# Kernel optimization log

Measured on AMD Instinct MI355X. Metric: run time of the kernel, lower is better.

The kernel has to match this reference:

```python
import jax, jax.numpy as jnp
import numpy as np

N = 8192      # num nodes
D = 256       # input feature dim (num_embeddings)
F_OUT = 128   # out_channels
B = 4096      # lookup batch size


def setup_inputs() -> dict:
    key = jax.random.key(0)
    k1, k2, k3, k4 = jax.random.split(key, 4)
    x = jax.random.randint(k1, (B,), 0, N)                      # node ids for final lookup
    adj = jax.random.randint(k2, (N, N), 0, 2).astype(jnp.int32)  # dense 0/1 adjacency
    embedding = jax.random.normal(k3, (N, D), dtype=jnp.float32)
    xavier = 1.414 * (6.0 / (D + F_OUT)) ** 0.5
    W = jax.random.uniform(k4, (D, F_OUT), minval=-xavier, maxval=xavier, dtype=jnp.float32)
    return {"x": x, "adj": adj, "embedding": embedding, "W": W}


def reference(x, adj, embedding, W):
    Wh = embedding @ W                                   # [N, F_OUT]
    mask = adj > 0
    maskf = mask.astype(Wh.dtype)
    # per-row neighbor mean of Wh (vectorized form of the python row loop)
    deg = jnp.maximum(jnp.sum(maskf, axis=1), 1.0)       # guard; random adj has deg>0
    neigh_mean = (maskf @ Wh) / deg[:, None]             # [N, F_OUT]
    alpha = jnp.sum(Wh * neigh_mean, axis=1)             # [N], Wh[i] . mean(neighbors)
    e = Wh @ Wh.T + alpha[:, None]                       # similarity + row-wise query term
    att = jax.nn.softmax(jnp.where(mask, e, jnp.asarray(-9e15, e.dtype)), axis=1)
    # dropout is identity in eval mode (p effectively 0)
    h_prime = att @ Wh                                   # [N, F_OUT]
    emb_out = jax.nn.elu(h_prime)                        # concat=True branch
    out = emb_out[x]                                     # F.embedding lookup, [B, F_OUT]
    nrm = jnp.linalg.norm(out, axis=1, keepdims=True)
    return out / jnp.maximum(nrm, 1e-12)                 # F.normalize (L2, eps=1e-12)
```

## Files before the change

kernel.cpp:

```cpp
#include <hip/hip_runtime.h>

#define NN 8192
#define DD 256
#define FF 128
#define BB 4096
#define NSPLIT 8
#define KCHUNK (NN / NSPLIT)
#define NITER (KCHUNK / 64)

typedef unsigned short ushortT;
typedef __attribute__((ext_vector_type(8))) short bf16x8;
typedef __attribute__((ext_vector_type(4))) float f32x4;

__device__ __forceinline__ ushortT f2bf(float f) {
  unsigned u = __float_as_uint(f);
  return (ushortT)((u + 0x7FFFu + ((u >> 16) & 1u)) >> 16);
}
__device__ __forceinline__ float bf2f(ushortT h) {
  return __uint_as_float(((unsigned)h) << 16);
}


__global__ __launch_bounds__(256) void init_kernel(int* flags, int* cnt) {
  int i = blockIdx.x * 256 + threadIdx.x;
  flags[i] = 0;
  if (i == 0) *cnt = 0;
}

__global__ __launch_bounds__(256) void scatter_kernel(const int* __restrict__ x, int* flags) {
  int b = blockIdx.x * 256 + threadIdx.x;
  flags[x[b]] = 1;
}

__global__ __launch_bounds__(256) void compact_kernel(const int* __restrict__ flags, int* cnt,
                                                      int* list, int* slot) {
  int i = blockIdx.x * 256 + threadIdx.x;
  if (flags[i]) {
    int pos = atomicAdd(cnt, 1);
    list[pos] = i;
    slot[i] = pos;
  }
}


__global__ __launch_bounds__(256) void pack_kernel(const int* __restrict__ adj,
                                                   const int* __restrict__ list,
                                                   const int* __restrict__ cntp,
                                                   unsigned* __restrict__ pk) {
  const int s = blockIdx.x >> 2;
  const int kc = (blockIdx.x & 3) * 2048;
  if (s >= *cntp) return;
  const int w = threadIdx.x >> 6, l = threadIdx.x & 63;
  const int* base = adj + (size_t)list[s] * NN + kc + w * 512;
  unsigned long long* dst = (unsigned long long*)(pk + s * 256 + (kc >> 5) + w * 16);
#pragma unroll
  for (int i = 0; i < 8; ++i) {
    unsigned long long b = __ballot(base[i * 64 + l] > 0);
    if (l == 0) dst[i] = b;
  }
}


__global__ __launch_bounds__(256) void wh_kernel(const float* __restrict__ emb,
                                                 const float* __restrict__ W,
                                                 ushortT* __restrict__ Whh,
                                                 ushortT* __restrict__ Whl) {
  __shared__ float Es[32 * 65];
  __shared__ float Ws[64 * 128];
  const int t = threadIdx.x;
  const int r0 = blockIdx.x * 32;
  const int rg = t >> 5;
  const int cg = t & 31;
  float4 acc[4] = {{0,0,0,0},{0,0,0,0},{0,0,0,0},{0,0,0,0}};
  for (int kc = 0; kc < DD; kc += 64) {
    __syncthreads();
    for (int i = 0; i < 8; ++i) {
      int idx = t + 256 * i;
      int r = idx >> 6, k = idx & 63;
      Es[r * 65 + k] = emb[(r0 + r) * DD + kc + k];
    }
    for (int i = 0; i < 8; ++i) {
      int idx = t + 256 * i;
      int kr = idx >> 5, c4 = (idx & 31) * 4;
      *(float4*)&Ws[kr * 128 + c4] = *(const float4*)&W[(kc + kr) * 128 + c4];
    }
    __syncthreads();
    for (int k = 0; k < 64; ++k) {
      float4 b = *(const float4*)&Ws[k * 128 + cg * 4];
#pragma unroll
      for (int i = 0; i < 4; ++i) {
        float a = Es[(rg * 4 + i) * 65 + k];
        acc[i].x += a * b.x; acc[i].y += a * b.y;
        acc[i].z += a * b.z; acc[i].w += a * b.w;
      }
    }
  }
#pragma unroll
  for (int i = 0; i < 4; ++i) {
    int row = r0 + rg * 4 + i;
    float v[4] = {acc[i].x, acc[i].y, acc[i].z, acc[i].w};
    ushort4 hh, ll;
    ushortT* hp = (ushortT*)&hh;
    ushortT* lp = (ushortT*)&ll;
#pragma unroll
    for (int k = 0; k < 4; ++k) {
      ushortT h = f2bf(v[k]);
      hp[k] = h;
      lp[k] = f2bf(v[k] - bf2f(h));
    }
    *(ushort4*)&Whh[row * FF + cg * 4] = hh;
    *(ushort4*)&Whl[row * FF + cg * 4] = ll;
  }
}


__global__ __launch_bounds__(256) void transpose_kernel(const ushortT* __restrict__ A,
                                                        ushortT* __restrict__ At) {
  __shared__ ushortT tile[64 * 72];
  const int t = threadIdx.x;
  const int r0 = (blockIdx.x >> 1) * 64, c0 = (blockIdx.x & 1) * 64;
#pragma unroll
  for (int i = 0; i < 2; ++i) {
    int idx = t + 256 * i;
    int r = idx >> 3, cb = idx & 7;
    *(bf16x8*)&tile[r * 72 + ((cb ^ ((r >> 3) & 7)) * 8)] =
        *(const bf16x8*)&A[(size_t)(r0 + r) * FF + c0 + cb * 8];
  }
  __syncthreads();
#pragma unroll
  for (int i = 0; i < 2; ++i) {
    int idx = t + 256 * i;
    int f = idx >> 3, r8 = idx & 7;
    bf16x8 v;
#pragma unroll
    for (int u = 0; u < 8; ++u) {
      int row = r8 * 8 + u;
      v[u] = (short)tile[row * 72 + (((f >> 3) ^ ((row >> 3) & 7)) * 8) + (f & 7)];
    }
    *(bf16x8*)&At[(size_t)(c0 + f) * NN + r0 + r8 * 8] = v;
  }
}


__global__ __launch_bounds__(256) void attn_kernel(
    const ushortT* __restrict__ Whh, const ushortT* __restrict__ Whl,
    const ushortT* __restrict__ WhT, const unsigned* __restrict__ pk,
    const int* __restrict__ list, const int* __restrict__ cntp,
    float* __restrict__ Opart, float* __restrict__ mpart, float* __restrict__ lpart) {
  __shared__ short Kh[2][64 * 128];
  __shared__ short Kl[2][64 * 128];
  __shared__ short Ps[4][16 * 72];
  __shared__ int nid[64];

  const int cnt = *cntp;
  const int qblk = blockIdx.x >> 3, chunk = blockIdx.x & 7;
  const int q0 = qblk * 64;
  if (q0 >= cnt) return;

  const int t = threadIdx.x;
  if (t < 64) nid[t] = list[min(q0 + t, cnt - 1)];
  __syncthreads();

  const int w = t >> 6, l = t & 63, quad = l >> 4, c = l & 15;

  const size_t qr = (size_t)nid[w * 16 + c] * FF;
  bf16x8 qh[4], ql[4];
#pragma unroll
  for (int ks = 0; ks < 4; ++ks) {
    qh[ks] = *(const bf16x8*)(Whh + qr + ks * 32 + quad * 8);
    ql[ks] = *(const bf16x8*)(Whl + qr + ks * 32 + quad * 8);
  }
  int prow[4];
#pragma unroll
  for (int r = 0; r < 4; ++r) prow[r] = min(q0 + w * 16 + quad * 4 + r, cnt - 1);

  float m[4], lr[4];
#pragma unroll
  for (int r = 0; r < 4; ++r) { m[r] = -1e30f; lr[r] = 0.f; }
  f32x4 O[8] = {{0,0,0,0},{0,0,0,0},{0,0,0,0},{0,0,0,0},
                {0,0,0,0},{0,0,0,0},{0,0,0,0},{0,0,0,0}};

  const int kt0 = chunk * KCHUNK;

  bf16x8 sgh[4], sgl[4];
  {
    const ushortT* gh = Whh + (size_t)kt0 * FF;
    const ushortT* gl = Whl + (size_t)kt0 * FF;
#pragma unroll
    for (int i = 0; i < 4; ++i) {
      int idx = t + 256 * i;
      sgh[i] = *(const bf16x8*)(gh + idx * 8);
      sgl[i] = *(const bf16x8*)(gl + idx * 8);
    }
#pragma unroll
    for (int i = 0; i < 4; ++i) {
      int idx = t + 256 * i;
      int r = idx >> 4, cb = idx & 15;
      int off = r * 128 + ((cb ^ (r & 7)) * 8);
      *(bf16x8*)&Kh[0][off] = sgh[i];
      *(bf16x8*)&Kl[0][off] = sgl[i];
    }
  }

  for (int it = 0; it < NITER; ++it) {
    const int kt = kt0 + it * 64;
    const int cur = it & 1;
    if (it + 1 < NITER) {
      const ushortT* gh = Whh + (size_t)(kt + 64) * FF;
      const ushortT* gl = Whl + (size_t)(kt + 64) * FF;
#pragma unroll
      for (int i = 0; i < 4; ++i) {
        int idx = t + 256 * i;
        sgh[i] = *(const bf16x8*)(gh + idx * 8);
        sgl[i] = *(const bf16x8*)(gl + idx * 8);
      }
    }
    unsigned mw0[4], mw1[4];
#pragma unroll
    for (int r = 0; r < 4; ++r) {
      uint2 mm = *(const uint2*)(pk + (size_t)prow[r] * 256 + (kt >> 5));
      mw0[r] = mm.x; mw1[r] = mm.y;
    }
    __syncthreads();

    f32x4 sacc[4];
#pragma unroll
    for (int nt = 0; nt < 4; ++nt) {
      const int rb = (nt * 16 + c) * 128;
      f32x4 a = {0, 0, 0, 0};
#pragma unroll
      for (int ks = 0; ks < 4; ++ks) {
        const int off = rb + (((ks * 4 + quad) ^ (c & 7)) * 8);
        bf16x8 bh = *(const bf16x8*)&Kh[cur][off];
        bf16x8 bl = *(const bf16x8*)&Kl[cur][off];
        a = __builtin_amdgcn_mfma_f32_16x16x32_bf16(qh[ks], bh, a, 0, 0, 0);
        a = __builtin_amdgcn_mfma_f32_16x16x32_bf16(ql[ks], bh, a, 0, 0, 0);
        a = __builtin_amdgcn_mfma_f32_16x16x32_bf16(qh[ks], bl, a, 0, 0, 0);
      }
      sacc[nt] = a;
    }

    float rmax[4];
#pragma unroll
    for (int r = 0; r < 4; ++r) {
      float v = -1e30f;
#pragma unroll
      for (int nt = 0; nt < 4; ++nt) {
        unsigned bit = ((nt < 2 ? mw0[r] : mw1[r]) >> ((nt & 1) * 16 + c)) & 1u;
        v = fmaxf(v, bit ? sacc[nt][r] : -1e30f);
      }
      rmax[r] = v;
    }
#pragma unroll
    for (int mk = 1; mk <= 8; mk <<= 1)
#pragma unroll
      for (int r = 0; r < 4; ++r) rmax[r] = fmaxf(rmax[r], __shfl_xor(rmax[r], mk, 16));
    float sc[4], psum[4];
#pragma unroll
    for (int r = 0; r < 4; ++r) {
      float nm = fmaxf(m[r], rmax[r]);
      sc[r] = __expf(m[r] - nm);
      m[r] = nm;
      psum[r] = 0.f;
    }
#pragma unroll
    for (int nt = 0; nt < 4; ++nt)
#pragma unroll
      for (int r = 0; r < 4; ++r) {
        unsigned bit = ((nt < 2 ? mw0[r] : mw1[r]) >> ((nt & 1) * 16 + c)) & 1u;
        float p = bit ? __expf(sacc[nt][r] - m[r]) : 0.f;
        ushortT pb = f2bf(p);
        Ps[w][(quad * 4 + r) * 72 + nt * 16 + c] = (short)pb;
        psum[r] += bf2f(pb);
      }
#pragma unroll
    for (int mk = 1; mk <= 8; mk <<= 1)
#pragma unroll
      for (int r = 0; r < 4; ++r) psum[r] += __shfl_xor(psum[r], mk, 16);
#pragma unroll
    for (int r = 0; r < 4; ++r) lr[r] = lr[r] * sc[r] + psum[r];

#pragma unroll
    for (int ft = 0; ft < 8; ++ft)
#pragma unroll
      for (int r = 0; r < 4; ++r) O[ft][r] *= sc[r];
    bf16x8 pa[2];
#pragma unroll
    for (int ks2 = 0; ks2 < 2; ++ks2)
      pa[ks2] = *(const bf16x8*)&Ps[w][c * 72 + ks2 * 32 + quad * 8];
#pragma unroll
    for (int ft = 0; ft < 8; ++ft) {
      const ushortT* vp = WhT + (size_t)(ft * 16 + c) * NN + kt + quad * 8;
#pragma unroll
      for (int ks2 = 0; ks2 < 2; ++ks2) {
        bf16x8 vb = *(const bf16x8*)(vp + ks2 * 32);
        O[ft] = __builtin_amdgcn_mfma_f32_16x16x32_bf16(pa[ks2], vb, O[ft], 0, 0, 0);
      }
    }

    if (it + 1 < NITER) {
#pragma unroll
      for (int i = 0; i < 4; ++i) {
        int idx = t + 256 * i;
        int r = idx >> 4, cb = idx & 15;
        int off = r * 128 + ((cb ^ (r & 7)) * 8);
        *(bf16x8*)&Kh[1 - cur][off] = sgh[i];
        *(bf16x8*)&Kl[1 - cur][off] = sgl[i];
      }
    }
  }

  float* Op = Opart + (size_t)chunk * 4096 * FF;
#pragma unroll
  for (int ft = 0; ft < 8; ++ft)
#pragma unroll
    for (int r = 0; r < 4; ++r)
      Op[(size_t)(q0 + w * 16 + quad * 4 + r) * FF + ft * 16 + c] = O[ft][r];
  if (c == 0) {
#pragma unroll
    for (int r = 0; r < 4; ++r) {
      mpart[chunk * 4096 + q0 + w * 16 + quad * 4 + r] = m[r];
      lpart[chunk * 4096 + q0 + w * 16 + quad * 4 + r] = lr[r];
    }
  }
}


__global__ __launch_bounds__(128) void combine_kernel(
    const float* __restrict__ Opart, const float* __restrict__ mpart,
    const float* __restrict__ lpart, float* __restrict__ h) {
  const int r = blockIdx.x;
  const int t = threadIdx.x;
  float mstar = -1e30f;
#pragma unroll
  for (int c = 0; c < NSPLIT; ++c) mstar = fmaxf(mstar, mpart[c * 4096 + r]);
  float lstar = 0.f, acc = 0.f;
#pragma unroll
  for (int c = 0; c < NSPLIT; ++c) {
    float wgt = __expf(mpart[c * 4096 + r] - mstar);
    lstar += wgt * lpart[c * 4096 + r];
    acc += wgt * Opart[((size_t)c * 4096 + r) * FF + t];
  }
  float v = acc / fmaxf(lstar, 1e-30f);
  h[r * FF + t] = v > 0.f ? v : expm1f(v);
}


__global__ __launch_bounds__(128) void out_kernel(const int* __restrict__ x,
                                                  const int* __restrict__ slot,
                                                  const float* __restrict__ h,
                                                  float* __restrict__ out) {
  const int b = blockIdx.x, t = threadIdx.x;
  const int s = slot[x[b]];
  float v = h[s * FF + t];
  float ss = v * v;
#pragma unroll
  for (int wd = 1; wd <= 32; wd <<= 1) ss += __shfl_xor(ss, wd);
  __shared__ float red[2];
  if ((t & 63) == 0) red[t >> 6] = ss;
  __syncthreads();
  float tot = red[0] + red[1];
  float scale = 1.f / fmaxf(sqrtf(tot), 1e-12f);
  out[b * FF + t] = v * scale;
}


extern "C" void kernel_launch(void* const* d_in, const int* in_sizes, int n_in,
                              void* d_out, int out_size, void* d_ws, size_t ws_size,
                              hipStream_t stream) {
  const int*   x   = (const int*)d_in[0];
  const int*   adj = (const int*)d_in[1];
  const float* emb = (const float*)d_in[2];
  const float* W   = (const float*)d_in[3];
  float* out = (float*)d_out;

  char* base = (char*)d_ws;
  ushortT* Whh = (ushortT*)(base);
  ushortT* Whl = (ushortT*)(base + 2097152);
  float*   h   = (float*)(base + 2097152);
  ushortT* WhT = (ushortT*)(base + 4194304);
  float* Opart = (float*)(base + 6291456);
  float* mpart = (float*)(base + 23068672);
  float* lpart = (float*)(base + 23199744);
  unsigned* pk = (unsigned*)(base + 23330816);
  int*   flags = (int*)(base + 27525120);
  int*   list  = (int*)(base + 27557888);
  int*   slot  = (int*)(base + 27574272);
  int*   cnt   = (int*)(base + 27607040);
  (void)in_sizes; (void)n_in; (void)out_size; (void)ws_size;

  hipLaunchKernelGGL(init_kernel,      dim3(NN / 256), dim3(256), 0, stream, flags, cnt);
  hipLaunchKernelGGL(scatter_kernel,   dim3(BB / 256), dim3(256), 0, stream, x, flags);
  hipLaunchKernelGGL(compact_kernel,   dim3(NN / 256), dim3(256), 0, stream, flags, cnt, list, slot);
  hipLaunchKernelGGL(pack_kernel,      dim3(4096 * 4), dim3(256), 0, stream, adj, list, cnt, pk);
  hipLaunchKernelGGL(wh_kernel,        dim3(NN / 32),  dim3(256), 0, stream, emb, W, Whh, Whl);
  hipLaunchKernelGGL(transpose_kernel, dim3((NN / 64) * 2), dim3(256), 0, stream, Whh, WhT);
  hipLaunchKernelGGL(attn_kernel,      dim3((BB / 64) * NSPLIT), dim3(256), 0, stream,
                     Whh, Whl, WhT, pk, list, cnt, Opart, mpart, lpart);
  hipLaunchKernelGGL(combine_kernel,   dim3(4096), dim3(128), 0, stream, Opart, mpart, lpart, h);
  hipLaunchKernelGGL(out_kernel,       dim3(BB),   dim3(128), 0, stream, x, slot, h, out);
}
```

Before: 463.8 us.

## Switch attention to fp16 split-precision, drop low key half, double key splits

Replaces the bf16 hi/lo split of Wh with fp16 hi/lo. The QK^T product now uses two MFMAs per step (q_hi·k_hi and q_lo·k_hi) instead of three, and the Kl shared-memory buffer and its global loads are removed. NSPLIT goes from 8 to 16 to give more blocks, launch_bounds now asks for 3 blocks per CU, and the workspace offsets grow to fit the larger partial buffers. Risks are fp16 range/overflow and lower key precision in the logits, plus more partial-result combine traffic.

After: 475.3 us. +2.5%, slower.

```diff
diff --git a/kernel.cpp b/kernel.cpp
--- a/kernel.cpp
+++ b/kernel.cpp
@@ -4,20 +4,20 @@
 #define DD 256
 #define FF 128
 #define BB 4096
-#define NSPLIT 8
+#define NSPLIT 16
 #define KCHUNK (NN / NSPLIT)
 #define NITER (KCHUNK / 64)
 
 typedef unsigned short ushortT;
-typedef __attribute__((ext_vector_type(8))) short bf16x8;
+typedef _Float16 f16;
+typedef __attribute__((ext_vector_type(8))) _Float16 f16x8;
 typedef __attribute__((ext_vector_type(4))) float f32x4;
 
-__device__ __forceinline__ ushortT f2bf(float f) {
-  unsigned u = __float_as_uint(f);
-  return (ushortT)((u + 0x7FFFu + ((u >> 16) & 1u)) >> 16);
-}
-__device__ __forceinline__ float bf2f(ushortT h) {
-  return __uint_as_float(((unsigned)h) << 16);
+__device__ __forceinline__ ushortT f2h_bits(float f) {
+  f16 h = (f16)f; ushortT u; __builtin_memcpy(&u, &h, 2); return u;
+}
+__device__ __forceinline__ float h_bits2f(ushortT u) {
+  f16 h; __builtin_memcpy(&h, &u, 2); return (float)h;
 }
 
 
@@ -104,9 +104,9 @@
     ushortT* lp = (ushortT*)&ll;
 #pragma unroll
     for (int k = 0; k < 4; ++k) {
-      ushortT h = f2bf(v[k]);
+      ushortT h = f2h_bits(v[k]);
       hp[k] = h;
-      lp[k] = f2bf(v[k] - bf2f(h));
+      lp[k] = f2h_bits(v[k] - h_bits2f(h));
     }
     *(ushort4*)&Whh[row * FF + cg * 4] = hh;
     *(ushort4*)&Whl[row * FF + cg * 4] = ll;
@@ -123,52 +123,68 @@
   for (int i = 0; i < 2; ++i) {
     int idx = t + 256 * i;
     int r = idx >> 3, cb = idx & 7;
-    *(bf16x8*)&tile[r * 72 + ((cb ^ ((r >> 3) & 7)) * 8)] =
-        *(const bf16x8*)&A[(size_t)(r0 + r) * FF + c0 + cb * 8];
+    *(ushort4*)&tile[r * 72 + ((cb ^ ((r >> 3) & 7)) * 8)] =
+        *(const ushort4*)&A[(size_t)(r0 + r) * FF + c0 + cb * 8];
+    *(ushort4*)&tile[r * 72 + ((cb ^ ((r >> 3) & 7)) * 8) + 4] =
+        *(const ushort4*)&A[(size_t)(r0 + r) * FF + c0 + cb * 8 + 4];
   }
   __syncthreads();
 #pragma unroll
   for (int i = 0; i < 2; ++i) {
     int idx = t + 256 * i;
     int f = idx >> 3, r8 = idx & 7;
-    bf16x8 v;
+    ushortT v[8];
 #pragma unroll
     for (int u = 0; u < 8; ++u) {
       int row = r8 * 8 + u;
-      v[u] = (short)tile[row * 72 + (((f >> 3) ^ ((row >> 3) & 7)) * 8) + (f & 7)];
-    }
-    *(bf16x8*)&At[(size_t)(c0 + f) * NN + r0 + r8 * 8] = v;
-  }
-}
-
-
-__global__ __launch_bounds__(256) void attn_kernel(
+      v[u] = tile[row * 72 + (((f >> 3) ^ ((row >> 3) & 7)) * 8) + (f & 7)];
+    }
+    *(ushort4*)&At[(size_t)(c0 + f) * NN + r0 + r8 * 8] = *(ushort4*)&v[0];
+    *(ushort4*)&At[(size_t)(c0 + f) * NN + r0 + r8 * 8 + 4] = *(ushort4*)&v[4];
+  }
+}
+
+
+__global__ __launch_bounds__(256, 3) void attn_kernel(
     const ushortT* __restrict__ Whh, const ushortT* __restrict__ Whl,
     const ushortT* __restrict__ WhT, const unsigned* __restrict__ pk,
     const int* __restrict__ list, const int* __restrict__ cntp,
     float* __restrict__ Opart, float* __restrict__ mpart, float* __restrict__ lpart) {
   __shared__ short Kh[2][64 * 128];
-  __shared__ short Kl[2][64 * 128];
   __shared__ short Ps[4][16 * 72];
   __shared__ int nid[64];
 
   const int cnt = *cntp;
-  const int qblk = blockIdx.x >> 3, chunk = blockIdx.x & 7;
+  const int qblk = blockIdx.x >> 4, chunk = blockIdx.x & 15;
   const int q0 = qblk * 64;
   if (q0 >= cnt) return;
 
   const int t = threadIdx.x;
   if (t < 64) nid[t] = list[min(q0 + t, cnt - 1)];
+  const int kt0 = chunk * KCHUNK;
+
+  f16x8 sg[4];
+#pragma unroll
+  for (int i = 0; i < 4; ++i) {
+    int idx = t + 256 * i;
+    sg[i] = *(const f16x8*)(Whh + (size_t)(kt0 + (idx >> 4)) * FF + (idx & 15) * 8);
+  }
   __syncthreads();
+#pragma unroll
+  for (int i = 0; i < 4; ++i) {
+    int idx = t + 256 * i;
+    int r = idx >> 4, cb = idx & 15;
+    *(f16x8*)&Kh[0][r * 128 + ((cb ^ (r & 7)) * 8)] = sg[i];
+  }
 
   const int w = t >> 6, l = t & 63, quad = l >> 4, c = l & 15;
 
   const size_t qr = (size_t)nid[w * 16 + c] * FF;
-  bf16x8 qh[4], ql[4];
+  f16x8 qh[4], ql[4];
 #pragma unroll
   for (int ks = 0; ks < 4; ++ks) {
-    qh[ks] = *(const bf16x8*)(Whh + qr + ks * 32 + quad * 8);
-    ql[ks] = *(const bf16x8*)(Whl + qr + ks * 32 + quad * 8);
+    qh[ks] = *(const f16x8*)(Whh + qr + ks * 32 + quad * 8);
+    ql[ks] = *(const f16x8*)(Whl + qr + ks * 32 + quad * 8);
   }
   int prow[4];
 #pragma unroll
@@ -180,48 +196,31 @@
   f32x4 O[8] = {{0,0,0,0},{0,0,0,0},{0,0,0,0},{0,0,0,0},
                 {0,0,0,0},{0,0,0,0},{0,0,0,0},{0,0,0,0}};
 
-  const int kt0 = chunk * KCHUNK;
-
-  bf16x8 sgh[4], sgl[4];
-  {
-    const ushortT* gh = Whh + (size_t)kt0 * FF;
-    const ushortT* gl = Whl + (size_t)kt0 * FF;
-#pragma unroll
-    for (int i = 0; i < 4; ++i) {
-      int idx = t + 256 * i;
-      sgh[i] = *(const bf16x8*)(gh + idx * 8);
-      sgl[i] = *(const bf16x8*)(gl + idx * 8);
-    }
-#pragma unroll
-    for (int i = 0; i < 4; ++i) {
-      int idx = t + 256 * i;
-      int r = idx >> 4, cb = idx & 15;
-      int off = r * 128 + ((cb ^ (r & 7)) * 8);
-      *(bf16x8*)&Kh[0][off] = sgh[i];
-      *(bf16x8*)&Kl[0][off] = sgl[i];
-    }
-  }
-
   for (int it = 0; it < NITER; ++it) {
     const int kt = kt0 + it * 64;
     const int cur = it & 1;
-    if (it + 1 < NITER) {
-      const ushortT* gh = Whh + (size_t)(kt + 64) * FF;
-      const ushortT* gl = Whl + (size_t)(kt + 64) * FF;
-#pragma unroll
-      for (int i = 0; i < 4; ++i) {
-        int idx = t + 256 * i;
-        sgh[i] = *(const bf16x8*)(gh + idx * 8);
-        sgl[i] = *(const bf16x8*)(gl + idx * 8);
-      }
-    }
     unsigned mw0[4], mw1[4];
 #pragma unroll
     for (int r = 0; r < 4; ++r) {
       uint2 mm = *(const uint2*)(pk + (size_t)prow[r] * 256 + (kt >> 5));
       mw0[r] = mm.x; mw1[r] = mm.y;
     }
+    if (it + 1 < NITER) {
+#pragma unroll
+      for (int i = 0; i < 4; ++i) {
+        int idx = t + 256 * i;
+        sg[i] = *(const f16x8*)(Whh + (size_t)(kt + 64 + (idx >> 4)) * FF + (idx & 15) * 8);
+      }
+    }
     __syncthreads();
+    if (it + 1 < NITER) {
+#pragma unroll
+      for (int i = 0; i < 4; ++i) {
+        int idx = t + 256 * i;
+        int r = idx >> 4, cb = idx & 15;
+        *(f16x8*)&Kh[1 - cur][r * 128 + ((cb ^ (r & 7)) * 8)] = sg[i];
+      }
+    }
 
     f32x4 sacc[4];
 #pragma unroll
@@ -231,11 +230,9 @@
 #pragma unroll
       for (int ks = 0; ks < 4; ++ks) {
         const int off = rb + (((ks * 4 + quad) ^ (c & 7)) * 8);
-        bf16x8 bh = *(const bf16x8*)&Kh[cur][off];
-        bf16x8 bl = *(const bf16x8*)&Kl[cur][off];
-        a = __builtin_amdgcn_mfma_f32_16x16x32_bf16(qh[ks], bh, a, 0, 0, 0);
-        a = __builtin_amdgcn_mfma_f32_16x16x32_bf16(ql[ks], bh, a, 0, 0, 0);
-        a = __builtin_amdgcn_mfma_f32_16x16x32_bf16(qh[ks], bl, a, 0, 0, 0);
+        f16x8 kv = *(const f16x8*)&Kh[cur][off];
+        a = __builtin_amdgcn_mfma_f32_16x16x32_f16(qh[ks], kv, a, 0, 0, 0);
+        a = __builtin_amdgcn_mfma_f32_16x16x32_f16(ql[ks], kv, a, 0, 0, 0);
       }
       sacc[nt] = a;
     }
@@ -269,9 +266,9 @@
       for (int r = 0; r < 4; ++r) {
         unsigned bit = ((nt < 2 ? mw0[r] : mw1[r]) >> ((nt & 1) * 16 + c)) & 1u;
         float p = bit ? __expf(sacc[nt][r] - m[r]) : 0.f;
-        ushortT pb = f2bf(p);
+        ushortT pb = f2h_bits(p);
         Ps[w][(quad * 4 + r) * 72 + nt * 16 + c] = (short)pb;
-        psum[r] += bf2f(pb);
+        psum[r] += h_bits2f(pb);
       }
 #pragma unroll
     for (int mk = 1; mk <= 8; mk <<= 1)
@@ -284,28 +281,17 @@
     for (int ft = 0; ft < 8; ++ft)
 #pragma unroll
       for (int r = 0; r < 4; ++r) O[ft][r] *= sc[r];
-    bf16x8 pa[2];
+    f16x8 pa[2];
 #pragma unroll
     for (int ks2 = 0; ks2 < 2; ++ks2)
-      pa[ks2] = *(const bf16x8*)&Ps[w][c * 72 + ks2 * 32 + quad * 8];
+      pa[ks2] = *(const f16x8*)&Ps[w][c * 72 + ks2 * 32 + quad * 8];
 #pragma unroll
     for (int ft = 0; ft < 8; ++ft) {
       const ushortT* vp = WhT + (size_t)(ft * 16 + c) * NN + kt + quad * 8;
 #pragma unroll
       for (int ks2 = 0; ks2 < 2; ++ks2) {
-        bf16x8 vb = *(const bf16x8*)(vp + ks2 * 32);
-        O[ft] = __builtin_amdgcn_mfma_f32_16x16x32_bf16(pa[ks2], vb, O[ft], 0, 0, 0);
-      }
-    }
-
-    if (it + 1 < NITER) {
-#pragma unroll
-      for (int i = 0; i < 4; ++i) {
-        int idx = t + 256 * i;
-        int r = idx >> 4, cb = idx & 15;
-        int off = r * 128 + ((cb ^ (r & 7)) * 8);
-        *(bf16x8*)&Kh[1 - cur][off] = sgh[i];
-        *(bf16x8*)&Kl[1 - cur][off] = sgl[i];
+        f16x8 vb = *(const f16x8*)(vp + ks2 * 32);
+        O[ft] = __builtin_amdgcn_mfma_f32_16x16x32_f16(pa[ks2], vb, O[ft], 0, 0, 0);
       }
     }
   }
@@ -380,13 +366,13 @@
   float*   h   = (float*)(base + 2097152);
   ushortT* WhT = (ushortT*)(base + 4194304);
   float* Opart = (float*)(base + 6291456);
-  float* mpart = (float*)(base + 23068672);
-  float* lpart = (float*)(base + 23199744);
-  unsigned* pk = (unsigned*)(base + 23330816);
-  int*   flags = (int*)(base + 27525120);
-  int*   list  = (int*)(base + 27557888);
-  int*   slot  = (int*)(base + 27574272);
-  int*   cnt   = (int*)(base + 27607040);
+  float* mpart = (float*)(base + 39845888);
+  float* lpart = (float*)(base + 40108032);
+  unsigned* pk = (unsigned*)(base + 40370176);
+  int*   flags = (int*)(base + 44564480);
+  int*   list  = (int*)(base + 44597248);
+  int*   slot  = (int*)(base + 44613632);
+  int*   cnt   = (int*)(base + 44646400);
   (void)in_sizes; (void)n_in; (void)out_size; (void)ws_size;
 
   hipLaunchKernelGGL(init_kernel,      dim3(NN / 256), dim3(256), 0, stream, flags, cnt);
```
